# Optimization experiments

Measured on AMD Instinct MI355X. Metric: run time of the kernel, lower is better.

The kernel has to match this reference:

```python
import jax, jax.numpy as jnp
import numpy as np

N_NODES = 10000
N_EDGES = 320000
HIDDEN = 256
HEADS = 8
HEAD_DIM = HIDDEN // HEADS  # 32
NEG_SLOPE = 0.2


def setup_inputs() -> dict:
    key = jax.random.key(0)
    ks = jax.random.split(key, 12)
    x = jax.random.normal(ks[0], (N_NODES, HIDDEN), dtype=jnp.float32)
    edges_idx = jax.random.randint(ks[1], (2, N_EDGES), 0, N_NODES, dtype=jnp.int64)
    s = 1.0 / np.sqrt(HIDDEN)
    # layer 1 params
    W1 = jax.random.normal(ks[2], (HIDDEN, HEADS * HEAD_DIM), dtype=jnp.float32) * s
    a_src1 = jax.random.normal(ks[3], (HEADS, HEAD_DIM), dtype=jnp.float32) * s
    a_dst1 = jax.random.normal(ks[4], (HEADS, HEAD_DIM), dtype=jnp.float32) * s
    b1 = jnp.zeros((HEADS * HEAD_DIM,), dtype=jnp.float32)
    # layer 2 params
    W2 = jax.random.normal(ks[5], (HIDDEN, HEADS * HEAD_DIM), dtype=jnp.float32) * s
    a_src2 = jax.random.normal(ks[6], (HEADS, HEAD_DIM), dtype=jnp.float32) * s
    a_dst2 = jax.random.normal(ks[7], (HEADS, HEAD_DIM), dtype=jnp.float32) * s
    b2 = jnp.zeros((HEADS * HEAD_DIM,), dtype=jnp.float32)
    return {"x": x, "edges_idx": edges_idx,
            "W1": W1, "a_src1": a_src1, "a_dst1": a_dst1, "b1": b1,
            "W2": W2, "a_src2": a_src2, "a_dst2": a_dst2, "b2": b2}


def gat_conv(x, src, dst, W, a_src, a_dst, b):
    """PyG GATConv (concat=True, negative_slope=0.2), dropout in eval mode."""
    N = x.shape[0]
    h = (x @ W).reshape(N, HEADS, HEAD_DIM)          # [N,H,C]
    alpha_s = jnp.einsum('nhc,hc->nh', h, a_src)     # [N,H]
    alpha_d = jnp.einsum('nhc,hc->nh', h, a_dst)     # [N,H]
    e = alpha_s[src] + alpha_d[dst]                  # [E,H]
    e = jnp.where(e > 0, e, NEG_SLOPE * e)           # leaky_relu
    # scatter-softmax over incoming edges of each dst node
    m = jax.ops.segment_max(e, dst, num_segments=N)  # [N,H]
    ex = jnp.exp(e - m[dst])                         # [E,H]
    denom = jax.ops.segment_sum(ex, dst, num_segments=N)  # [N,H]
    alpha = ex / (denom[dst] + 1e-16)                # [E,H]
    msg = h[src] * alpha[:, :, None]                 # [E,H,C]
    out = jax.ops.segment_sum(msg, dst, num_segments=N)   # [N,H,C]
    return out.reshape(N, HEADS * HEAD_DIM) + b


def reference(x, edges_idx, W1, a_src1, a_dst1, b1, W2, a_src2, a_dst2, b2):
    src = edges_idx[0]
    dst = edges_idx[1]
    h = gat_conv(x, src, dst, W1, a_src1, a_dst1, b1)
    h = jax.nn.elu(h)
    out = gat_conv(h, src, dst, W2, a_src2, a_dst2, b2)
    return out
```

## Files before the change

### kernel.cpp

```cpp
#include <hip/hip_runtime.h>
#include <hip/hip_bf16.h>
#include <hip/hip_fp16.h>

#define N_NODES 10000
#define N_EDGES 320000
#define HIDDEN 256
#define HEADS 8
#define HEAD_DIM 32
#define NEG_SLOPE 0.2f
#define CAP 80

typedef __attribute__((ext_vector_type(8))) short short8;
typedef __attribute__((ext_vector_type(8))) _Float16 half8;
typedef __attribute__((ext_vector_type(4))) float f32x4;

__device__ __forceinline__ void bf16_split(float v, unsigned short& hi, unsigned short& lo) {
    __hip_bfloat16 hb = __float2bfloat16(v);
    float hf = __bfloat162float(hb);
    __hip_bfloat16 lb = __float2bfloat16(v - hf);
    hi = *reinterpret_cast<unsigned short*>(&hb);
    lo = *reinterpret_cast<unsigned short*>(&lb);
}

__global__ __launch_bounds__(256) void prep_kernel(
    const float* __restrict__ W1, const float* __restrict__ W2,
    const int* __restrict__ src, const int* __restrict__ dst,
    unsigned short* __restrict__ w1h, unsigned short* __restrict__ w1l,
    unsigned short* __restrict__ w2h, unsigned short* __restrict__ w2l,
    int* __restrict__ counts, int* __restrict__ csr_src) {
    int b = blockIdx.x;
    int tid = threadIdx.x;
    if (b < 512) {
        int i = b * 256 + tid;
        int which = i >> 16;
        int rem = i & 0xFFFF;
        int k = rem >> 8, n = rem & 255;
        const float* W = which ? W2 : W1;
        unsigned short* wh = which ? w2h : w1h;
        unsigned short* wl = which ? w2l : w1l;
        unsigned short h, l;
        bf16_split(W[k * 256 + n], h, l);
        wh[n * 256 + k] = h;
        wl[n * 256 + k] = l;
    } else {
        int e = (b - 512) * 256 + tid;
        int d = dst[e];
        int rank = atomicAdd(&counts[d], 1);
        csr_src[d * CAP + rank] = src[e];
    }
}

template <int AFP32>
__global__ __launch_bounds__(512) void gemm_mfma_kernel(
    const float* __restrict__ Axf,
    const unsigned short* __restrict__ Ah, const unsigned short* __restrict__ Al,
    const unsigned short* __restrict__ BhT, const unsigned short* __restrict__ BlT,
    _Float16* __restrict__ hH, const float* __restrict__ a_src,
    const float* __restrict__ a_dst, float* __restrict__ alpha_s,
    float* __restrict__ alpha_d) {
    __shared__ __align__(16) char smem[42240];
    unsigned short* sAh = (unsigned short*)smem;
    unsigned short* sAl = (unsigned short*)(smem + 6400);
    unsigned short* sBh = (unsigned short*)(smem + 12800);
    unsigned short* sBl = (unsigned short*)(smem + 23040);
    _Float16* sOut = (_Float16*)smem;

    const int tid = threadIdx.x;
    const int w = tid >> 6, lane = tid & 63;
    const int c = w & 3, g = w >> 2;
    const int rtbase = g ? 3 : 0, nrt = g ? 2 : 3;
    const int col = lane & 15, quad = lane >> 4;
    const int m0 = blockIdx.y * 80, n0 = blockIdx.x * 128;

    f32x4 acc[3][2] = {};
    float4 raf[2][2];
    uint4 rau[2][2];
    uint4 rb[2][2];

#define LOAD_A(k0, SS)                                                          \
    if (AFP32) {                                                                \
        _Pragma("unroll") for (int i = 0; i < 2; ++i) {                         \
            int t = tid + i * 512;                                              \
            if (t < 640) {                                                      \
                int row = t >> 3, seg = t & 7;                                  \
                raf[SS][i] = *(const float4*)&Axf[(size_t)(m0 + row) * 256 + (k0) + seg * 4]; \
            }                                                                   \
        }                                                                       \
    } else {                                                                    \
        _Pragma("unroll") for (int i = 0; i < 2; ++i) {                         \
            int t = tid + i * 512;                                              \
            if (t < 640) {                                                      \
                int tt = t < 320 ? t : t - 320;                                 \
                int row = tt >> 2, seg = tt & 3;                                \
                const unsigned short* P = t < 320 ? Ah : Al;                    \
                rau[SS][i] = *(const uint4*)&P[(size_t)(m0 + row) * 256 + (k0) + seg * 8]; \
            }                                                                   \
        }                                                                       \
    }
#define LOAD_B(k0, SS)                                                          \
    _Pragma("unroll") for (int i = 0; i < 2; ++i) {                             \
        int t = tid + i * 512;                                                  \
        int tt = t < 512 ? t : t - 512;                                         \
        int row = tt >> 2, seg = tt & 3;                                        \
        const unsigned short* P = t < 512 ? BhT : BlT;                          \
        rb[SS][i] = *(const uint4*)&P[(size_t)(n0 + row) * 256 + (k0) + seg * 8]; \
    }
#define WRITE_A(SS)                                                             \
    if (AFP32) {                                                                \
        _Pragma("unroll") for (int i = 0; i < 2; ++i) {                         \
            int t = tid + i * 512;                                              \
            if (t < 640) {                                                      \
                int row = t >> 3, seg = t & 7;                                  \
                float4 v = raf[SS][i];                                          \
                ushort4 hh, ll;                                                 \
                unsigned short hb, lb;                                          \
                bf16_split(v.x, hb, lb); hh.x = hb; ll.x = lb;                  \
                bf16_split(v.y, hb, lb); hh.y = hb; ll.y = lb;                  \
                bf16_split(v.z, hb, lb); hh.z = hb; ll.z = lb;                  \
                bf16_split(v.w, hb, lb); hh.w = hb; ll.w = lb;                  \
                *(ushort4*)&sAh[row * 40 + seg * 4] = hh;                       \
                *(ushort4*)&sAl[row * 40 + seg * 4] = ll;                       \
            }                                                                   \
        }                                                                       \
    } else {                                                                    \
        _Pragma("unroll") for (int i = 0; i < 2; ++i) {                         \
            int t = tid + i * 512;                                              \
            if (t < 640) {                                                      \
                int tt = t < 320 ? t : t - 320;                                 \
                int row = tt >> 2, seg = tt & 3;                                \
                unsigned short* Sp = t < 320 ? sAh : sAl;                       \
                *(uint4*)&Sp[row * 40 + seg * 8] = rau[SS][i];                  \
            }                                                                   \
        }                                                                       \
    }
#define WRITE_B(SS)                                                             \
    _Pragma("unroll") for (int i = 0; i < 2; ++i) {                             \
        int t = tid + i * 512;                                                  \
        int tt = t < 512 ? t : t - 512;                                         \
        int row = tt >> 2, seg = tt & 3;                                        \
        unsigned short* Sp = t < 512 ? sBh : sBl;                               \
        *(uint4*)&Sp[row * 40 + seg * 8] = rb[SS][i];                           \
    }

    LOAD_A(0, 0)
    LOAD_B(0, 0)
    LOAD_A(32, 1)
    LOAD_B(32, 1)

#pragma unroll
    for (int ks = 0; ks < 8; ++ks) {
        WRITE_A(ks & 1)
        WRITE_B(ks & 1)
        __syncthreads();

        if (ks < 6) {
            LOAD_A((ks + 2) * 32, ks & 1)
            LOAD_B((ks + 2) * 32, ks & 1)
        }

        short8 bh0 = *(const short8*)&sBh[(c * 32 + col) * 40 + quad * 8];
        short8 bl0 = *(const short8*)&sBl[(c * 32 + col) * 40 + quad * 8];
        short8 bh1 = *(const short8*)&sBh[(c * 32 + 16 + col) * 40 + quad * 8];
        short8 bl1 = *(const short8*)&sBl[(c * 32 + 16 + col) * 40 + quad * 8];
#pragma unroll
        for (int rt = 0; rt < 3; ++rt) {
            if (rt < nrt) {
                int rg = rtbase + rt;
                short8 ah = *(const short8*)&sAh[(rg * 16 + col) * 40 + quad * 8];
                short8 al = *(const short8*)&sAl[(rg * 16 + col) * 40 + quad * 8];
                acc[rt][0] = __builtin_amdgcn_mfma_f32_16x16x32_bf16(ah, bh0, acc[rt][0], 0, 0, 0);
                acc[rt][0] = __builtin_amdgcn_mfma_f32_16x16x32_bf16(ah, bl0, acc[rt][0], 0, 0, 0);
                acc[rt][0] = __builtin_amdgcn_mfma_f32_16x16x32_bf16(al, bh0, acc[rt][0], 0, 0, 0);
                acc[rt][1] = __builtin_amdgcn_mfma_f32_16x16x32_bf16(ah, bh1, acc[rt][1], 0, 0, 0);
                acc[rt][1] = __builtin_amdgcn_mfma_f32_16x16x32_bf16(ah, bl1, acc[rt][1], 0, 0, 0);
                acc[rt][1] = __builtin_amdgcn_mfma_f32_16x16x32_bf16(al, bh1, acc[rt][1], 0, 0, 0);
            }
        }
        __syncthreads();
    }
#undef LOAD_A
#undef LOAD_B
#undef WRITE_A
#undef WRITE_B

    const int head = blockIdx.x * 4 + c;
    float as0 = a_src[n0 + c * 32 + col];
    float as1 = a_src[n0 + c * 32 + 16 + col];
    float ad0 = a_dst[n0 + c * 32 + col];
    float ad1 = a_dst[n0 + c * 32 + 16 + col];
#pragma unroll
    for (int rt = 0; rt < 3; ++rt) {
        if (rt < nrt) {
            int rg = rtbase + rt;
#pragma unroll
            for (int r = 0; r < 4; ++r) {
                int row = rg * 16 + quad * 4 + r;
                sOut[row * 264 + c * 32 + col]      = (_Float16)acc[rt][0][r];
                sOut[row * 264 + c * 32 + 16 + col] = (_Float16)acc[rt][1][r];
                float ps = acc[rt][0][r] * as0 + acc[rt][1][r] * as1;
                float pd = acc[rt][0][r] * ad0 + acc[rt][1][r] * ad1;
#pragma unroll
                for (int m = 1; m < 16; m <<= 1) {
                    ps += __shfl_xor(ps, m);
                    pd += __shfl_xor(pd, m);
                }
                if (col == 0) {
                    int gm = m0 + row;
                    alpha_s[gm * HEADS + head] = ps;
                    alpha_d[gm * HEADS + head] = pd;
                }
            }
        }
    }
    __syncthreads();
#pragma unroll
    for (int i = 0; i < 3; ++i) {
        int t = tid + i * 512;
        if (t < 1280) {
            int row = t >> 4, seg = t & 15;
            *(half8*)&hH[(size_t)(m0 + row) * 256 + n0 + seg * 8] =
                *(const half8*)&sOut[row * 264 + seg * 8];
        }
    }
}

__global__ __launch_bounds__(256) void aggregate_kernel(
    const int* __restrict__ counts, const int* __restrict__ csr_src,
    const float* __restrict__ alpha_s, const float* __restrict__ alpha_d,
    const _Float16* __restrict__ hH, const float* __restrict__ bias,
    float* __restrict__ outf, unsigned short* __restrict__ oh,
    unsigned short* __restrict__ ol, int mode) {
    const int tid = threadIdx.x;
    const int w = tid >> 6, lane = tid & 63;
    const int ph = blockIdx.x / 2500;
    const int d = (blockIdx.x - ph * 2500) * 4 + w;
    const int q = lane >> 4, fl = lane & 15;
    const int hd = ph * 4 + (fl >> 2);
    const int qb = q * 4;
    const int* __restrict__ bucket = csr_src + d * CAP;
    const _Float16* hp = hH + ph * 128 + fl * 8;

    const int n = counts[d];
    const float ad = alpha_d[d * HEADS + hd];
    int4 s0_ = *(const int4*)&bucket[qb];
    int4 s1_ = *(const int4*)&bucket[qb + 16];
    int4 s2_ = *(const int4*)&bucket[qb + 32];
    int4 s3_ = *(const int4*)&bucket[qb + 48];

    float acc[8] = {};
    float den = 0.f;

#define AGG_DECL(t) float al##t##0, al##t##1, al##t##2, al##t##3;               \
                    half8 hv##t##0, hv##t##1, hv##t##2, hv##t##3;
    AGG_DECL(0) AGG_DECL(1) AGG_DECL(2) AGG_DECL(3) AGG_DECL(4)

#define AGG_CLAMP(x) ((x) < 0 ? 0 : ((x) > 9999 ? 9999 : (x)))
#define AGG_GATHER(t, sv)                                                       \
    {                                                                           \
        int i0_ = AGG_CLAMP((sv).x), i1_ = AGG_CLAMP((sv).y);                   \
        int i2_ = AGG_CLAMP((sv).z), i3_ = AGG_CLAMP((sv).w);                   \
        al##t##0 = alpha_s[i0_ * HEADS + hd];                                   \
        al##t##1 = alpha_s[i1_ * HEADS + hd];                                   \
        al##t##2 = alpha_s[i2_ * HEADS + hd];                                   \
        al##t##3 = alpha_s[i3_ * HEADS + hd];                                   \
        hv##t##0 = *(const half8*)&hp[(size_t)i0_ * HIDDEN];                    \
        hv##t##1 = *(const half8*)&hp[(size_t)i1_ * HIDDEN];                    \
        hv##t##2 = *(const half8*)&hp[(size_t)i2_ * HIDDEN];                    \
        hv##t##3 = *(const half8*)&hp[(size_t)i3_ * HIDDEN];                    \
    }
#define AGG_COMPUTE(t, base)                                                    \
    {                                                                           \
        int b0_ = (base) + qb;                                                  \
        float e0 = al##t##0 + ad; e0 = e0 > 0.f ? e0 : NEG_SLOPE * e0;          \
        float e1 = al##t##1 + ad; e1 = e1 > 0.f ? e1 : NEG_SLOPE * e1;          \
        float e2 = al##t##2 + ad; e2 = e2 > 0.f ? e2 : NEG_SLOPE * e2;          \
        float e3 = al##t##3 + ad; e3 = e3 > 0.f ? e3 : NEG_SLOPE * e3;          \
        if (b0_ >= n)     e0 = -1e30f;                                          \
        if (b0_ + 1 >= n) e1 = -1e30f;                                          \
        if (b0_ + 2 >= n) e2 = -1e30f;                                          \
        if (b0_ + 3 >= n) e3 = -1e30f;                                          \
        float ev0 = __expf(e0), ev1 = __expf(e1);                               \
        float ev2 = __expf(e2), ev3 = __expf(e3);                               \
        den += (ev0 + ev1) + (ev2 + ev3);                                       \
        _Pragma("unroll") for (int j = 0; j < 8; ++j)                           \
            acc[j] += (float)hv##t##0[j] * ev0 + (float)hv##t##1[j] * ev1 +     \
                      (float)hv##t##2[j] * ev2 + (float)hv##t##3[j] * ev3;      \
    }

    if (n > 0)  AGG_GATHER(0, s0_)
    if (n > 16) AGG_GATHER(1, s1_)
    if (n > 0)  AGG_COMPUTE(0, 0)
    if (n > 32) AGG_GATHER(2, s2_)
    if (n > 16) AGG_COMPUTE(1, 16)
    if (n > 48) AGG_GATHER(3, s3_)
    if (n > 32) AGG_COMPUTE(2, 32)
    if (n > 48) AGG_COMPUTE(3, 48)
    if (n > 64) {
        int4 s4_ = *(const int4*)&bucket[qb + 64];
        AGG_GATHER(4, s4_)
        AGG_COMPUTE(4, 64)
    }

#undef AGG_DECL
#undef AGG_CLAMP
#undef AGG_GATHER
#undef AGG_COMPUTE

#pragma unroll
    for (int j = 0; j < 8; ++j) acc[j] += __shfl_xor(acc[j], 16);
    den += __shfl_xor(den, 16);
#pragma unroll
    for (int j = 0; j < 8; ++j) acc[j] += __shfl_xor(acc[j], 32);
    den += __shfl_xor(den, 32);

    if (q == 0) {
        float inv = 1.f / (den + 1e-16f);
        float v[8];
#pragma unroll
        for (int j = 0; j < 8; ++j)
            v[j] = acc[j] * inv + bias[ph * 128 + fl * 8 + j];
        size_t oidx = (size_t)d * HIDDEN + ph * 128 + fl * 8;
        if (mode == 1) {
            unsigned short hb[8], lb[8];
#pragma unroll
            for (int j = 0; j < 8; ++j) {
                v[j] = v[j] > 0.f ? v[j] : (__expf(v[j]) - 1.f);
                bf16_split(v[j], hb[j], lb[j]);
            }
            *(ushort4*)&oh[oidx]     = make_ushort4(hb[0], hb[1], hb[2], hb[3]);
            *(ushort4*)&oh[oidx + 4] = make_ushort4(hb[4], hb[5], hb[6], hb[7]);
            *(ushort4*)&ol[oidx]     = make_ushort4(lb[0], lb[1], lb[2], lb[3]);
            *(ushort4*)&ol[oidx + 4] = make_ushort4(lb[4], lb[5], lb[6], lb[7]);
        } else {
            *(float4*)&outf[oidx]     = make_float4(v[0], v[1], v[2], v[3]);
            *(float4*)&outf[oidx + 4] = make_float4(v[4], v[5], v[6], v[7]);
        }
    }
}

extern "C" void kernel_launch(void* const* d_in, const int* in_sizes, int n_in,
                              void* d_out, int out_size, void* d_ws, size_t ws_size,
                              hipStream_t stream) {
    const float* x      = (const float*)d_in[0];
    const int*   edges  = (const int*)d_in[1];
    const float* W1     = (const float*)d_in[2];
    const float* as1    = (const float*)d_in[3];
    const float* ad1    = (const float*)d_in[4];
    const float* b1     = (const float*)d_in[5];
    const float* W2     = (const float*)d_in[6];
    const float* as2    = (const float*)d_in[7];
    const float* ad2    = (const float*)d_in[8];
    const float* b2     = (const float*)d_in[9];
    float* out = (float*)d_out;

    const int* src = edges;
    const int* dst = edges + N_EDGES;

    const size_t NF = (size_t)N_NODES * HIDDEN;
    const size_t NH = (size_t)N_NODES * HEADS;

    char* base = (char*)d_ws;
    _Float16* hH = (_Float16*)base;             base += NF * 2;
    unsigned short* x2h = (unsigned short*)base; base += NF * 2;
    unsigned short* x2l = (unsigned short*)base; base += NF * 2;
    float* alpha_s = (float*)base;              base += NH * 4;
    float* alpha_d = (float*)base;              base += NH * 4;
    unsigned short* w1h = (unsigned short*)base; base += 65536 * 2;
    unsigned short* w1l = (unsigned short*)base; base += 65536 * 2;
    unsigned short* w2h = (unsigned short*)base; base += 65536 * 2;
    unsigned short* w2l = (unsigned short*)base; base += 65536 * 2;
    int* csr_src = (int*)base;                  base += (size_t)N_NODES * CAP * 4;
    int* counts  = (int*)base;                  base += (size_t)N_NODES * 4;

    dim3 gemm_grid(2, 125);
    const int EB = (N_EDGES + 255) / 256;
    const int AGG_B = 2500 * 2;

    hipMemsetAsync(counts, 0, N_NODES * sizeof(int), stream);
    prep_kernel<<<512 + EB, 256, 0, stream>>>(W1, W2, src, dst,
                                              w1h, w1l, w2h, w2l, counts, csr_src);

    gemm_mfma_kernel<1><<<gemm_grid, 512, 0, stream>>>(
        x, nullptr, nullptr, w1h, w1l, hH, as1, ad1, alpha_s, alpha_d);
    aggregate_kernel<<<AGG_B, 256, 0, stream>>>(counts, csr_src, alpha_s, alpha_d,
                                                hH, b1, nullptr, x2h, x2l, 1);

    gemm_mfma_kernel<0><<<gemm_grid, 512, 0, stream>>>(
        nullptr, x2h, x2l, w2h, w2l, hH, as2, ad2, alpha_s, alpha_d);
    aggregate_kernel<<<AGG_B, 256, 0, stream>>>(counts, csr_src, alpha_s, alpha_d,
                                                hH, b2, out, nullptr, nullptr, 0);
}
```

Measured before the change: 189.1 us.

## Preload full B tile into LDS and merge aggregate head halves per wave

```diff
diff --git a/kernel.cpp b/kernel.cpp
--- a/kernel.cpp
+++ b/kernel.cpp
@@ -58,12 +58,12 @@
     _Float16* __restrict__ hH, const float* __restrict__ a_src,
     const float* __restrict__ a_dst, float* __restrict__ alpha_s,
     float* __restrict__ alpha_d) {
-    __shared__ __align__(16) char smem[42240];
+    __shared__ __align__(16) char smem[147968];
     unsigned short* sAh = (unsigned short*)smem;
     unsigned short* sAl = (unsigned short*)(smem + 6400);
     unsigned short* sBh = (unsigned short*)(smem + 12800);
-    unsigned short* sBl = (unsigned short*)(smem + 23040);
-    _Float16* sOut = (_Float16*)smem;
+    unsigned short* sBl = (unsigned short*)(smem + 80384);
+    _Float16* sOut = (_Float16*)(smem + 12800);
 
     const int tid = threadIdx.x;
     const int w = tid >> 6, lane = tid & 63;
@@ -75,7 +75,6 @@
     f32x4 acc[3][2] = {};
     float4 raf[2][2];
     uint4 rau[2][2];
-    uint4 rb[2][2];
 
 #define LOAD_A(k0, SS)                                                          \
     if (AFP32) {                                                                \
@@ -96,14 +95,6 @@
                 rau[SS][i] = *(const uint4*)&P[(size_t)(m0 + row) * 256 + (k0) + seg * 8]; \
             }                                                                   \
         }                                                                       \
-    }
-#define LOAD_B(k0, SS)                                                          \
-    _Pragma("unroll") for (int i = 0; i < 2; ++i) {                             \
-        int t = tid + i * 512;                                                  \
-        int tt = t < 512 ? t : t - 512;                                         \
-        int row = tt >> 2, seg = tt & 3;                                        \
-        const unsigned short* P = t < 512 ? BhT : BlT;                          \
-        rb[SS][i] = *(const uint4*)&P[(size_t)(n0 + row) * 256 + (k0) + seg * 8]; \
     }
 #define WRITE_A(SS)                                                             \
     if (AFP32) {                                                                \
@@ -133,35 +124,42 @@
             }                                                                   \
         }                                                                       \
     }
-#define WRITE_B(SS)                                                             \
-    _Pragma("unroll") for (int i = 0; i < 2; ++i) {                             \
-        int t = tid + i * 512;                                                  \
-        int tt = t < 512 ? t : t - 512;                                         \
-        int row = tt >> 2, seg = tt & 3;                                        \
-        unsigned short* Sp = t < 512 ? sBh : sBl;                               \
-        *(uint4*)&Sp[row * 40 + seg * 8] = rb[SS][i];                           \
-    }
 
     LOAD_A(0, 0)
-    LOAD_B(0, 0)
     LOAD_A(32, 1)
-    LOAD_B(32, 1)
+
+    {
+        uint4 rbh[8], rbl[8];
+#pragma unroll
+        for (int i = 0; i < 8; ++i) {
+            int chunk = tid + i * 512;
+            int row = chunk >> 5, ks8 = chunk & 31;
+            rbh[i] = *(const uint4*)&BhT[(size_t)(n0 + row) * 256 + ks8 * 8];
+            rbl[i] = *(const uint4*)&BlT[(size_t)(n0 + row) * 256 + ks8 * 8];
+        }
+#pragma unroll
+        for (int i = 0; i < 8; ++i) {
+            int chunk = tid + i * 512;
+            int row = chunk >> 5, ks8 = chunk & 31;
+            *(uint4*)&sBh[row * 264 + ks8 * 8] = rbh[i];
+            *(uint4*)&sBl[row * 264 + ks8 * 8] = rbl[i];
+        }
+    }
 
 #pragma unroll
     for (int ks = 0; ks < 8; ++ks) {
         WRITE_A(ks & 1)
-        WRITE_B(ks & 1)
         __syncthreads();
 
         if (ks < 6) {
             LOAD_A((ks + 2) * 32, ks & 1)
-            LOAD_B((ks + 2) * 32, ks & 1)
-        }
-
-        short8 bh0 = *(const short8*)&sBh[(c * 32 + col) * 40 + quad * 8];
-        short8 bl0 = *(const short8*)&sBl[(c * 32 + col) * 40 + quad * 8];
-        short8 bh1 = *(const short8*)&sBh[(c * 32 + 16 + col) * 40 + quad * 8];
-        short8 bl1 = *(const short8*)&sBl[(c * 32 + 16 + col) * 40 + quad * 8];
+        }
+
+        const int kb = ks * 32 + quad * 8;
+        short8 bh0 = *(const short8*)&sBh[(c * 32 + col) * 264 + kb];
+        short8 bl0 = *(const short8*)&sBl[(c * 32 + col) * 264 + kb];
+        short8 bh1 = *(const short8*)&sBh[(c * 32 + 16 + col) * 264 + kb];
+        short8 bl1 = *(const short8*)&sBl[(c * 32 + 16 + col) * 264 + kb];
 #pragma unroll
         for (int rt = 0; rt < 3; ++rt) {
             if (rt < nrt) {
@@ -179,9 +177,7 @@
         __syncthreads();
     }
 #undef LOAD_A
-#undef LOAD_B
 #undef WRITE_A
-#undef WRITE_B
 
     const int head = blockIdx.x * 4 + c;
     float as0 = a_src[n0 + c * 32 + col];
@@ -232,26 +228,29 @@
     unsigned short* __restrict__ ol, int mode) {
     const int tid = threadIdx.x;
     const int w = tid >> 6, lane = tid & 63;
-    const int ph = blockIdx.x / 2500;
-    const int d = (blockIdx.x - ph * 2500) * 4 + w;
+    const int d = blockIdx.x * 4 + w;
     const int q = lane >> 4, fl = lane & 15;
-    const int hd = ph * 4 + (fl >> 2);
+    const int hd0 = fl >> 2, hd1 = 4 + (fl >> 2);
     const int qb = q * 4;
     const int* __restrict__ bucket = csr_src + d * CAP;
-    const _Float16* hp = hH + ph * 128 + fl * 8;
+    const _Float16* hp0 = hH + fl * 8;
+    const _Float16* hp1 = hH + 128 + fl * 8;
 
     const int n = counts[d];
-    const float ad = alpha_d[d * HEADS + hd];
+    const float ad0 = alpha_d[d * HEADS + hd0];
+    const float ad1 = alpha_d[d * HEADS + hd1];
     int4 s0_ = *(const int4*)&bucket[qb];
     int4 s1_ = *(const int4*)&bucket[qb + 16];
     int4 s2_ = *(const int4*)&bucket[qb + 32];
     int4 s3_ = *(const int4*)&bucket[qb + 48];
 
-    float acc[8] = {};
-    float den = 0.f;
-
-#define AGG_DECL(t) float al##t##0, al##t##1, al##t##2, al##t##3;               \
-                    half8 hv##t##0, hv##t##1, hv##t##2, hv##t##3;
+    float accA[8] = {}, accB[8] = {};
+    float denA = 0.f, denB = 0.f;
+
+#define AGG_DECL(t) float aA##t##0, aA##t##1, aA##t##2, aA##t##3;               \
+                    float aB##t##0, aB##t##1, aB##t##2, aB##t##3;               \
+                    half8 hA##t##0, hA##t##1, hA##t##2, hA##t##3;               \
+                    half8 hB##t##0, hB##t##1, hB##t##2, hB##t##3;
     AGG_DECL(0) AGG_DECL(1) AGG_DECL(2) AGG_DECL(3) AGG_DECL(4)
 
 #define AGG_CLAMP(x) ((x) < 0 ? 0 : ((x) > 9999 ? 9999 : (x)))
@@ -259,32 +258,50 @@
     {                                                                           \
         int i0_ = AGG_CLAMP((sv).x), i1_ = AGG_CLAMP((sv).y);                   \
         int i2_ = AGG_CLAMP((sv).z), i3_ = AGG_CLAMP((sv).w);                   \
-        al##t##0 = alpha_s[i0_ * HEADS + hd];                                   \
-        al##t##1 = alpha_s[i1_ * HEADS + hd];                                   \
-        al##t##2 = alpha_s[i2_ * HEADS + hd];                                   \
-        al##t##3 = alpha_s[i3_ * HEADS + hd];                                   \
-        hv##t##0 = *(const half8*)&hp[(size_t)i0_ * HIDDEN];                    \
-        hv##t##1 = *(const half8*)&hp[(size_t)i1_ * HIDDEN];                    \
-        hv##t##2 = *(const half8*)&hp[(size_t)i2_ * HIDDEN];                    \
-        hv##t##3 = *(const half8*)&hp[(size_t)i3_ * HIDDEN];                    \
+        aA##t##0 = alpha_s[i0_ * HEADS + hd0];                                  \
+        aA##t##1 = alpha_s[i1_ * HEADS + hd0];                                  \
+        aA##t##2 = alpha_s[i2_ * HEADS + hd0];                                  \
+        aA##t##3 = alpha_s[i3_ * HEADS + hd0];                                  \
+        aB##t##0 = alpha_s[i0_ * HEADS + hd1];                                  \
+        aB##t##1 = alpha_s[i1_ * HEADS + hd1];                                  \
+        aB##t##2 = alpha_s[i2_ * HEADS + hd1];                                  \
+        aB##t##3 = alpha_s[i3_ * HEADS + hd1];                                  \
+        hA##t##0 = *(const half8*)&hp0[(size_t)i0_ * HIDDEN];                   \
+        hA##t##1 = *(const half8*)&hp0[(size_t)i1_ * HIDDEN];                   \
+        hA##t##2 = *(const half8*)&hp0[(size_t)i2_ * HIDDEN];                   \
+        hA##t##3 = *(const half8*)&hp0[(size_t)i3_ * HIDDEN];                   \
+        hB##t##0 = *(const half8*)&hp1[(size_t)i0_ * HIDDEN];                   \
+        hB##t##1 = *(const half8*)&hp1[(size_t)i1_ * HIDDEN];                   \
+        hB##t##2 = *(const half8*)&hp1[(size_t)i2_ * HIDDEN];                   \
+        hB##t##3 = *(const half8*)&hp1[(size_t)i3_ * HIDDEN];                   \
     }
 #define AGG_COMPUTE(t, base)                                                    \
     {                                                                           \
         int b0_ = (base) + qb;                                                  \
-        float e0 = al##t##0 + ad; e0 = e0 > 0.f ? e0 : NEG_SLOPE * e0;          \
-        float e1 = al##t##1 + ad; e1 = e1 > 0.f ? e1 : NEG_SLOPE * e1;          \
-        float e2 = al##t##2 + ad; e2 = e2 > 0.f ? e2 : NEG_SLOPE * e2;          \
-        float e3 = al##t##3 + ad; e3 = e3 > 0.f ? e3 : NEG_SLOPE * e3;          \
-        if (b0_ >= n)     e0 = -1e30f;                                          \
-        if (b0_ + 1 >= n) e1 = -1e30f;                                          \
-        if (b0_ + 2 >= n) e2 = -1e30f;                                          \
-        if (b0_ + 3 >= n) e3 = -1e30f;                                          \
-        float ev0 = __expf(e0), ev1 = __expf(e1);                               \
-        float ev2 = __expf(e2), ev3 = __expf(e3);                               \
-        den += (ev0 + ev1) + (ev2 + ev3);                                       \
+        float eA0 = aA##t##0 + ad0; eA0 = eA0 > 0.f ? eA0 : NEG_SLOPE * eA0;    \
+        float eA1 = aA##t##1 + ad0; eA1 = eA1 > 0.f ? eA1 : NEG_SLOPE * eA1;    \
+        float eA2 = aA##t##2 + ad0; eA2 = eA2 > 0.f ? eA2 : NEG_SLOPE * eA2;    \
+        float eA3 = aA##t##3 + ad0; eA3 = eA3 > 0.f ? eA3 : NEG_SLOPE * eA3;    \
+        float eB0 = aB##t##0 + ad1; eB0 = eB0 > 0.f ? eB0 : NEG_SLOPE * eB0;    \
+        float eB1 = aB##t##1 + ad1; eB1 = eB1 > 0.f ? eB1 : NEG_SLOPE * eB1;    \
+        float eB2 = aB##t##2 + ad1; eB2 = eB2 > 0.f ? eB2 : NEG_SLOPE * eB2;    \
+        float eB3 = aB##t##3 + ad1; eB3 = eB3 > 0.f ? eB3 : NEG_SLOPE * eB3;    \
+        if (b0_ >= n)     { eA0 = -1e30f; eB0 = -1e30f; }                       \
+        if (b0_ + 1 >= n) { eA1 = -1e30f; eB1 = -1e30f; }                       \
+        if (b0_ + 2 >= n) { eA2 = -1e30f; eB2 = -1e30f; }                       \
+        if (b0_ + 3 >= n) { eA3 = -1e30f; eB3 = -1e30f; }                       \
+        float vA0 = __expf(eA0), vA1 = __expf(eA1);                             \
+        float vA2 = __expf(eA2), vA3 = __expf(eA3);                             \
+        float vB0 = __expf(eB0), vB1 = __expf(eB1);                             \
+        float vB2 = __expf(eB2), vB3 = __expf(eB3);                             \
+        denA += (vA0 + vA1) + (vA2 + vA3);                                      \
+        denB += (vB0 + vB1) + (vB2 + vB3);                                      \
         _Pragma("unroll") for (int j = 0; j < 8; ++j)                           \
-            acc[j] += (float)hv##t##0[j] * ev0 + (float)hv##t##1[j] * ev1 +     \
-                      (float)hv##t##2[j] * ev2 + (float)hv##t##3[j] * ev3;      \
+            accA[j] += (float)hA##t##0[j] * vA0 + (float)hA##t##1[j] * vA1 +    \
+                       (float)hA##t##2[j] * vA2 + (float)hA##t##3[j] * vA3;     \
+        _Pragma("unroll") for (int j = 0; j < 8; ++j)                           \
+            accB[j] += (float)hB##t##0[j] * vB0 + (float)hB##t##1[j] * vB1 +    \
+                       (float)hB##t##2[j] * vB2 + (float)hB##t##3[j] * vB3;     \
     }
 
     if (n > 0)  AGG_GATHER(0, s0_)
@@ -307,33 +324,56 @@
 #undef AGG_COMPUTE
 
 #pragma unroll
-    for (int j = 0; j < 8; ++j) acc[j] += __shfl_xor(acc[j], 16);
-    den += __shfl_xor(den, 16);
-#pragma unroll
-    for (int j = 0; j < 8; ++j) acc[j] += __shfl_xor(acc[j], 32);
-    den += __shfl_xor(den, 32);
+    for (int j = 0; j < 8; ++j) {
+        accA[j] += __shfl_xor(accA[j], 16);
+        accB[j] += __shfl_xor(accB[j], 16);
+    }
+    denA += __shfl_xor(denA, 16);
+    denB += __shfl_xor(denB, 16);
+#pragma unroll
+    for (int j = 0; j < 8; ++j) {
+        accA[j] += __shfl_xor(accA[j], 32);
+        accB[j] += __shfl_xor(accB[j], 32);
+    }
+    denA += __shfl_xor(denA, 32);
+    denB += __shfl_xor(denB, 32);
 
     if (q == 0) {
-        float inv = 1.f / (den + 1e-16f);
-        float v[8];
-#pragma unroll
-        for (int j = 0; j < 8; ++j)
-            v[j] = acc[j] * inv + bias[ph * 128 + fl * 8 + j];
-        size_t oidx = (size_t)d * HIDDEN + ph * 128 + fl * 8;
+        float invA = 1.f / (denA + 1e-16f);
+        float invB = 1.f / (denB + 1e-16f);
+        float vA[8], vB[8];
+#pragma unroll
+        for (int j = 0; j < 8; ++j) {
+            vA[j] = accA[j] * invA + bias[fl * 8 + j];
+            vB[j] = accB[j] * invB + bias[128 + fl * 8 + j];
+        }
+        size_t o0 = (size_t)d * HIDDEN + fl * 8;
+        size_t o1 = o0 + 128;
         if (mode == 1) {
             unsigned short hb[8], lb[8];
 #pragma unroll
             for (int j = 0; j < 8; ++j) {
-                v[j] = v[j] > 0.f ? v[j] : (__expf(v[j]) - 1.f);
-                bf16_split(v[j], hb[j], lb[j]);
+                vA[j] = vA[j] > 0.f ? vA[j] : (__expf(vA[j]) - 1.f);
+                bf16_split(vA[j], hb[j], lb[j]);
             }
-            *(ushort4*)&oh[oidx]     = make_ushort4(hb[0], hb[1], hb[2], hb[3]);
-            *(ushort4*)&oh[oidx + 4] = make_ushort4(hb[4], hb[5], hb[6], hb[7]);
-            *(ushort4*)&ol[oidx]     = make_ushort4(lb[0], lb[1], lb[2], lb[3]);
-            *(ushort4*)&ol[oidx + 4] = make_ushort4(lb[4], lb[5], lb[6], lb[7]);
+            *(ushort4*)&oh[o0]     = make_ushort4(hb[0], hb[1], hb[2], hb[3]);
+            *(ushort4*)&oh[o0 + 4] = make_ushort4(hb[4], hb[5], hb[6], hb[7]);
+            *(ushort4*)&ol[o0]     = make_ushort4(lb[0], lb[1], lb[2], lb[3]);
+            *(ushort4*)&ol[o0 + 4] = make_ushort4(lb[4], lb[5], lb[6], lb[7]);
+#pragma unroll
+            for (int j = 0; j < 8; ++j) {
+                vB[j] = vB[j] > 0.f ? vB[j] : (__expf(vB[j]) - 1.f);
+                bf16_split(vB[j], hb[j], lb[j]);
+            }
+            *(ushort4*)&oh[o1]     = make_ushort4(hb[0], hb[1], hb[2], hb[3]);
+            *(ushort4*)&oh[o1 + 4] = make_ushort4(hb[4], hb[5], hb[6], hb[7]);
+            *(ushort4*)&ol[o1]     = make_ushort4(lb[0], lb[1], lb[2], lb[3]);
+            *(ushort4*)&ol[o1 + 4] = make_ushort4(lb[4], lb[5], lb[6], lb[7]);
         } else {
-            *(float4*)&outf[oidx]     = make_float4(v[0], v[1], v[2], v[3]);
-            *(float4*)&outf[oidx + 4] = make_float4(v[4], v[5], v[6], v[7]);
+            *(float4*)&outf[o0]     = make_float4(vA[0], vA[1], vA[2], vA[3]);
+            *(float4*)&outf[o0 + 4] = make_float4(vA[4], vA[5], vA[6], vA[7]);
+            *(float4*)&outf[o1]     = make_float4(vB[0], vB[1], vB[2], vB[3]);
+            *(float4*)&outf[o1 + 4] = make_float4(vB[4], vB[5], vB[6], vB[7]);
         }
     }
 }
@@ -374,7 +414,7 @@
 
     dim3 gemm_grid(2, 125);
     const int EB = (N_EDGES + 255) / 256;
-    const int AGG_B = 2500 * 2;
+    const int AGG_B = 2500;
 
     hipMemsetAsync(counts, 0, N_NODES * sizeof(int), stream);
     prep_kernel<<<512 + EB, 256, 0, stream>>>(W1, W2, src, dst,
```

After: 181.0 us. 1.04x faster.
